# Kernel tuning notes

Measured on AMD Instinct MI355X. Metric: run time of the kernel, lower is better.

The kernel has to match this reference:

```python
import jax, jax.numpy as jnp
import numpy as np


def to_tb(r, size, base=4):
    # (B, size, size, size) -> (B, (size//base)^3, base, base, base)
    n = size // base
    r = r.reshape(-1, size, size, n, base)
    r = r.transpose(0, 1, 3, 2, 4)
    r = r.reshape(-1, size, n * n, base, base)
    r = r.transpose(0, 2, 1, 3, 4)
    return r.reshape(-1, n ** 3, base, base, base)


def from_tb(r, size, base=4):
    # inverse-ish of to_tb, ends with an extra (0,1,3,2) transpose as in source
    n = size // base
    r = r.reshape(-1, n * n, size, base, base)
    r = r.transpose(0, 2, 1, 3, 4)
    r = r.reshape(-1, size, size, n, base)
    r = r.transpose(0, 1, 3, 2, 4)
    r = r.reshape(-1, size, size, size)
    return r.transpose(0, 1, 3, 2)


def downscale(r, size):
    r = to_tb(r, size)  # base=4
    r = r.sum(axis=(2, 3, 4)) / 64.0
    r = r.reshape(-1, size // 4, size // 4, size // 4)
    return r.transpose(0, 3, 2, 1)


def setup_inputs() -> dict:
    key = jax.random.key(0)
    # (batch=2, level=4, 4, 4, 4^(3*4-2)) with 4*4*1048576 = 256^3 per slice
    x = jax.random.normal(key, (2, 4, 4, 4, 1048576), dtype=jnp.float32)
    return {"x": x}


def reference(x):
    level = x.shape[1]
    xt = jnp.transpose(x, (1, 0, 2, 3, 4))  # (level, batch, 4, 4, ...)
    batch = xt.shape[1]
    d2 = xt.shape[2]
    size_full = 4 ** level
    n3 = (4 ** (level - 1)) ** 3
    ret = []
    for i in range(level):
        r = xt[i]
        r = from_tb(r, size_full, 4 ** i)  # -> (batch, size, size, size)
        for k in range(i):
            r = downscale(r, 4 ** (level - k))
        for _ in range(i):
            r = jnp.tile(r, (1, 4, 4, 4))
        r = to_tb(r, size_full)  # (batch, n3, 4, 4, 4)
        ret.append(r.reshape(-1, n3, 64))
    out = jnp.stack(ret)  # (level, batch, n3, 64)
    out = out.transpose(1, 0, 2, 3).reshape(batch, -1, d2 ** 3)
    return out
```

## Files before the change

kernel.cpp:

```cpp
#include <hip/hip_runtime.h>


typedef float f4 __attribute__((ext_vector_type(4)));

__global__ __launch_bounds__(256) void k_reduce(const float* __restrict__ in,
                                                float* __restrict__ d1,
                                                float* __restrict__ p2,
                                                float* __restrict__ p3) {
    const int b = blockIdx.y;
    const int bx = blockIdx.x;
    const int tid = threadIdx.x;
    __shared__ float red[64];
    const f4* in4 = (const f4*)in;

    if (bx < 1024) {
        const int tlow = bx;
        const long base4 = (long)b * 16777216 + 4194304;
        float acc[4] = {0.f, 0.f, 0.f, 0.f};
        for (int dz = 0; dz < 4; ++dz) {
            long rb = base4 + (long)(dz * 1024 + tlow) * 1024;
#pragma unroll
            for (int k = 0; k < 4; ++k) {
                f4 v = __builtin_nontemporal_load(&in4[rb + k * 256 + tid]);
                acc[k] += v.x + v.y + v.z + v.w;
            }
        }
#pragma unroll
        for (int k = 0; k < 4; ++k) {
            acc[k] += __shfl_xor(acc[k], 4);
            acc[k] += __shfl_xor(acc[k], 8);
        }
        if ((tid & 12) == 0) {
            int yp = tlow >> 4;
            int zp = ((tlow & 15) << 2) + (tid & 3);
#pragma unroll
            for (int k = 0; k < 4; ++k) {
                int xp = k * 16 + (tid >> 4);
                int f4i = (zp >> 2) * 4096 + (yp >> 2) * 256 +
                          (xp >> 2) * 16 + (xp & 3) * 4 + (yp & 3);
                d1[b * 262144 + f4i * 4 + (zp & 3)] = acc[k] * (1.0f / 64.0f);
            }
        }
    } else if (bx < 2048) {
        const int blk = bx - 1024;
        const int g = blk & 3, cell = blk >> 2;
        const int yp = cell >> 4, xp = cell & 15;
        const long base4 = (long)b * 16777216 + 2 * 4194304 + yp * 16384 + xp * 1024;
        float acc = 0.f;
        for (int dzi = 0; dzi < 4; ++dzi) {
            long rb = base4 + (long)(g * 4 + dzi) * 262144;
#pragma unroll
            for (int k = 0; k < 4; ++k) {
                f4 v = __builtin_nontemporal_load(&in4[rb + k * 256 + tid]);
                acc += v.x + v.y + v.z + v.w;
            }
        }
        acc += __shfl_xor(acc, 1);
        acc += __shfl_xor(acc, 2);
        if ((tid & 3) == 0) red[tid >> 2] = acc;
        __syncthreads();
        if (tid < 16) {
            float s = red[tid] + red[16 + tid] + red[32 + tid] + red[48 + tid];
            p2[(b * 4 + g) * 4096 + xp * 256 + yp * 16 + tid] = s;
        }
    } else {
        const int blk = bx - 2048;
        const int kc = blk & 3;
        const int orig = blk >> 2;
        const int xp = orig >> 6, hi = (orig >> 2) & 15, dxg = orig & 3;
        const long base4 = (long)b * 16777216 + 3 * 4194304 +
                           (long)hi * 262144 + xp * 65536 + dxg * 16384;
        float acc = 0.f;
        for (int kk = 0; kk < 16; ++kk) {
            f4 v = __builtin_nontemporal_load(&in4[base4 + (kc * 16 + kk) * 256 + tid]);
            acc += v.x + v.y + v.z + v.w;
        }
        acc += __shfl_xor(acc, 1);
        acc += __shfl_xor(acc, 2);
        acc += __shfl_xor(acc, 4);
        acc += __shfl_xor(acc, 8);
        if ((tid & 15) == 0) red[tid >> 4] = acc;
        __syncthreads();
        if (tid < 16) {
            int G = (hi * 4 + dxg) * 4 + kc;
            p3[((b * 4 + xp) * 256 + G) * 16 + tid] = red[tid];
        }
    }
}

__global__ __launch_bounds__(256) void k_write(const float* __restrict__ in,
                                               const float* __restrict__ d1,
                                               const float* __restrict__ p2,
                                               const float* __restrict__ p3,
                                               float* __restrict__ out) {
    const int b = blockIdx.y;
    const int bx = blockIdx.x;
    const int tid = threadIdx.x;
    __shared__ f4 smem4[1040];
    f4* out4 = (f4*)out;

    if (bx < 4096) {
        float* smem = (float*)smem4;
        const f4* in4 = (const f4*)in;
        const int Y_hi = bx >> 6, Z_hi = bx & 63;
        const long in_b4 = (long)b * 16777216;
#pragma unroll
        for (int k = 0; k < 4; ++k) {
            int idx = k * 256 + tid;
            int r = idx >> 6, col4 = idx & 63;
            int Y = Y_hi * 4 + (r >> 2), Z = Z_hi * 4 + (r & 3);
            f4 v = __builtin_nontemporal_load(&in4[in_b4 + (long)Y * 16384 + Z * 64 + col4]);
            *(f4*)&smem[r * 260 + col4 * 4] = v;
        }
        __syncthreads();
        const long out_b4 = (long)b * 16777216 + (long)Z_hi * 65536 + Y_hi * 1024;
#pragma unroll
        for (int k = 0; k < 4; ++k) {
            int idx = k * 256 + tid;
            int X = ((idx >> 4) << 2) + ((tid >> 2) & 3);
            int row0 = (tid & 3) * 4;
            f4 v;
            v.x = smem[(row0 + 0) * 260 + X];
            v.y = smem[(row0 + 1) * 260 + X];
            v.z = smem[(row0 + 2) * 260 + X];
            v.w = smem[(row0 + 3) * 260 + X];
            __builtin_nontemporal_store(v, &out4[out_b4 + idx]);
        }
    } else if (bx < 6144) {
        const int blk = bx - 4096;
        const f4* d14 = (const f4*)d1;
        const int bx0 = blk * 2;
        const int base = b * 65536 + ((bx0 >> 6) & 15) * 4096 + (bx0 & 15) * 256 + tid;
        const f4 v0 = d14[base];
        const f4 v1 = d14[base + 256];
        const long ob = (long)b * 16777216 + 4194304 + (long)blk * 2048;
#pragma unroll
        for (int j = 0; j < 8; ++j)
            __builtin_nontemporal_store((j < 4) ? v0 : v1, &out4[ob + j * 256 + tid]);
    } else if (bx < 8192) {
        const int blk = bx - 6144;
        const f4* p24 = (const f4*)p2;
        const int bx0 = blk * 2;
        const int t6 = tid & 63;
        const int xp = ((t6 >> 4) << 2) + ((t6 >> 2) & 3);
        const int ylo = t6 & 3;
        f4 v01[2];
#pragma unroll
        for (int r = 0; r < 2; ++r) {
            int row = bx0 + r;
            int zq = (row >> 6) & 3, yq = row & 3;
            int yp = yq * 4 + ylo;
            f4 s = {0.f, 0.f, 0.f, 0.f};
#pragma unroll
            for (int g = 0; g < 4; ++g)
                s += p24[(b * 4 + g) * 1024 + xp * 64 + yp * 4 + zq];
            v01[r] = s * (1.0f / 4096.0f);
        }
        const long ob = (long)b * 16777216 + 2 * 4194304 + (long)blk * 2048;
#pragma unroll
        for (int j = 0; j < 8; ++j)
            __builtin_nontemporal_store((j < 4) ? v01[0] : v01[1],
                                        &out4[ob + j * 256 + tid]);
    } else {
        const int blk = bx - 8192;
        const f4* p34 = (const f4*)p3;
        const int o = tid & 15, part = tid >> 4;
        const int xp = o >> 2, cq = o & 3;
        f4 s = {0.f, 0.f, 0.f, 0.f};
#pragma unroll
        for (int j = 0; j < 16; ++j) {
            int G = part * 16 + j;
            s += p34[((b * 4 + xp) * 256 + G) * 4 + cq];
        }
        f4* red = smem4;
        red[part * 16 + o] = s;
        __syncthreads();
        f4* tab = smem4 + 256;
        if (tid < 16) {
            f4 t = {0.f, 0.f, 0.f, 0.f};
#pragma unroll
            for (int g = 0; g < 16; ++g) t += red[g * 16 + tid];
            tab[tid] = t * (1.0f / 262144.0f);
        }
        __syncthreads();
        const f4 v = tab[tid & 15];
        const long ob = (long)b * 16777216 + 3 * 4194304 + (long)blk * 8192;
#pragma unroll
        for (int j = 0; j < 32; ++j)
            __builtin_nontemporal_store(v, &out4[ob + j * 256 + tid]);
    }
}

extern "C" void kernel_launch(void* const* d_in, const int* in_sizes, int n_in,
                              void* d_out, int out_size, void* d_ws, size_t ws_size,
                              hipStream_t stream) {
    const float* in = (const float*)d_in[0];
    float* out = (float*)d_out;
    float* ws = (float*)d_ws;
    float* d1 = ws;
    float* p2 = ws + 524288;
    float* p3 = ws + 524288 + 65536;
    k_reduce<<<dim3(3072, 2), 256, 0, stream>>>(in, d1, p2, p3);
    k_write <<<dim3(8704, 2), 256, 0, stream>>>(in, d1, p2, p3, out);
}
```

Measured before the change: 186.6 us.

## Move level-0 transpose copy into reduce kernel, split broadcast writes into second kernel

The level-0 transpose-copy blocks move from the write kernel into the first kernel, so the whole input-read phase (reductions plus the transposing copy) runs in one launch. The second kernel now holds only the broadcast-fill blocks that read the small partial-sum buffers. The read-heavy and write-heavy work is rebalanced across the two launches, and the biggest broadcast blocks are scheduled first. Reduction blocks are also interleaved by batch instead of using a 2D grid. The cost is a larger shared allocation in the fused first kernel, which may lower its occupancy.

```diff
diff --git a/kernel.cpp b/kernel.cpp
--- a/kernel.cpp
+++ b/kernel.cpp
@@ -3,106 +3,100 @@
 
 typedef float f4 __attribute__((ext_vector_type(4)));
 
-__global__ __launch_bounds__(256) void k_reduce(const float* __restrict__ in,
-                                                float* __restrict__ d1,
-                                                float* __restrict__ p2,
-                                                float* __restrict__ p3) {
-    const int b = blockIdx.y;
+__global__ __launch_bounds__(256) void k_read(const float* __restrict__ in,
+                                              float* __restrict__ out,
+                                              float* __restrict__ d1,
+                                              float* __restrict__ p2,
+                                              float* __restrict__ p3) {
     const int bx = blockIdx.x;
     const int tid = threadIdx.x;
-    __shared__ float red[64];
+    __shared__ float smem[16 * 260];
     const f4* in4 = (const f4*)in;
 
-    if (bx < 1024) {
-        const int tlow = bx;
-        const long base4 = (long)b * 16777216 + 4194304;
-        float acc[4] = {0.f, 0.f, 0.f, 0.f};
-        for (int dz = 0; dz < 4; ++dz) {
-            long rb = base4 + (long)(dz * 1024 + tlow) * 1024;
+    if (bx < 6144) {
+        const int b = bx & 1;
+        const int rbx = bx >> 1;
+        float* red = smem;
+
+        if (rbx < 1024) {
+            const int tlow = rbx;
+            const long base4 = (long)b * 16777216 + 4194304;
+            float acc[4] = {0.f, 0.f, 0.f, 0.f};
+            for (int dz = 0; dz < 4; ++dz) {
+                long rb = base4 + (long)(dz * 1024 + tlow) * 1024;
+#pragma unroll
+                for (int k = 0; k < 4; ++k) {
+                    f4 v = __builtin_nontemporal_load(&in4[rb + k * 256 + tid]);
+                    acc[k] += v.x + v.y + v.z + v.w;
+                }
+            }
 #pragma unroll
             for (int k = 0; k < 4; ++k) {
-                f4 v = __builtin_nontemporal_load(&in4[rb + k * 256 + tid]);
-                acc[k] += v.x + v.y + v.z + v.w;
-            }
-        }
-#pragma unroll
-        for (int k = 0; k < 4; ++k) {
-            acc[k] += __shfl_xor(acc[k], 4);
-            acc[k] += __shfl_xor(acc[k], 8);
-        }
-        if ((tid & 12) == 0) {
-            int yp = tlow >> 4;
-            int zp = ((tlow & 15) << 2) + (tid & 3);
-#pragma unroll
-            for (int k = 0; k < 4; ++k) {
-                int xp = k * 16 + (tid >> 4);
-                int f4i = (zp >> 2) * 4096 + (yp >> 2) * 256 +
-                          (xp >> 2) * 16 + (xp & 3) * 4 + (yp & 3);
-                d1[b * 262144 + f4i * 4 + (zp & 3)] = acc[k] * (1.0f / 64.0f);
-            }
-        }
-    } else if (bx < 2048) {
-        const int blk = bx - 1024;
-        const int g = blk & 3, cell = blk >> 2;
-        const int yp = cell >> 4, xp = cell & 15;
-        const long base4 = (long)b * 16777216 + 2 * 4194304 + yp * 16384 + xp * 1024;
-        float acc = 0.f;
-        for (int dzi = 0; dzi < 4; ++dzi) {
-            long rb = base4 + (long)(g * 4 + dzi) * 262144;
-#pragma unroll
-            for (int k = 0; k < 4; ++k) {
-                f4 v = __builtin_nontemporal_load(&in4[rb + k * 256 + tid]);
+                acc[k] += __shfl_xor(acc[k], 4);
+                acc[k] += __shfl_xor(acc[k], 8);
+            }
+            if ((tid & 12) == 0) {
+                int yp = tlow >> 4;
+                int zp = ((tlow & 15) << 2) + (tid & 3);
+#pragma unroll
+                for (int k = 0; k < 4; ++k) {
+                    int xp = k * 16 + (tid >> 4);
+                    int f4i = (zp >> 2) * 4096 + (yp >> 2) * 256 +
+                              (xp >> 2) * 16 + (xp & 3) * 4 + (yp & 3);
+                    d1[b * 262144 + f4i * 4 + (zp & 3)] = acc[k] * (1.0f / 64.0f);
+                }
+            }
+        } else if (rbx < 2048) {
+            const int blk = rbx - 1024;
+            const int g = blk & 3, cell = blk >> 2;
+            const int yp = cell >> 4, xp = cell & 15;
+            const long base4 = (long)b * 16777216 + 2 * 4194304 + yp * 16384 + xp * 1024;
+            float acc = 0.f;
+            for (int dzi = 0; dzi < 4; ++dzi) {
+                long rb = base4 + (long)(g * 4 + dzi) * 262144;
+#pragma unroll
+                for (int k = 0; k < 4; ++k) {
+                    f4 v = __builtin_nontemporal_load(&in4[rb + k * 256 + tid]);
+                    acc += v.x + v.y + v.z + v.w;
+                }
+            }
+            acc += __shfl_xor(acc, 1);
+            acc += __shfl_xor(acc, 2);
+            if ((tid & 3) == 0) red[tid >> 2] = acc;
+            __syncthreads();
+            if (tid < 16) {
+                float s = red[tid] + red[16 + tid] + red[32 + tid] + red[48 + tid];
+                p2[(b * 4 + g) * 4096 + xp * 256 + yp * 16 + tid] = s;
+            }
+        } else {
+            const int blk = rbx - 2048;
+            const int kc = blk & 3;
+            const int orig = blk >> 2;
+            const int xp = orig >> 6, hi = (orig >> 2) & 15, dxg = orig & 3;
+            const long base4 = (long)b * 16777216 + 3 * 4194304 +
+                               (long)hi * 262144 + xp * 65536 + dxg * 16384;
+            float acc = 0.f;
+            for (int kk = 0; kk < 16; ++kk) {
+                f4 v = __builtin_nontemporal_load(&in4[base4 + (kc * 16 + kk) * 256 + tid]);
                 acc += v.x + v.y + v.z + v.w;
             }
-        }
-        acc += __shfl_xor(acc, 1);
-        acc += __shfl_xor(acc, 2);
-        if ((tid & 3) == 0) red[tid >> 2] = acc;
-        __syncthreads();
-        if (tid < 16) {
-            float s = red[tid] + red[16 + tid] + red[32 + tid] + red[48 + tid];
-            p2[(b * 4 + g) * 4096 + xp * 256 + yp * 16 + tid] = s;
+            acc += __shfl_xor(acc, 1);
+            acc += __shfl_xor(acc, 2);
+            acc += __shfl_xor(acc, 4);
+            acc += __shfl_xor(acc, 8);
+            if ((tid & 15) == 0) red[tid >> 4] = acc;
+            __syncthreads();
+            if (tid < 16) {
+                int G = (hi * 4 + dxg) * 4 + kc;
+                p3[((b * 4 + xp) * 256 + G) * 16 + tid] = red[tid];
+            }
         }
     } else {
-        const int blk = bx - 2048;
-        const int kc = blk & 3;
-        const int orig = blk >> 2;
-        const int xp = orig >> 6, hi = (orig >> 2) & 15, dxg = orig & 3;
-        const long base4 = (long)b * 16777216 + 3 * 4194304 +
-                           (long)hi * 262144 + xp * 65536 + dxg * 16384;
-        float acc = 0.f;
-        for (int kk = 0; kk < 16; ++kk) {
-            f4 v = __builtin_nontemporal_load(&in4[base4 + (kc * 16 + kk) * 256 + tid]);
-            acc += v.x + v.y + v.z + v.w;
-        }
-        acc += __shfl_xor(acc, 1);
-        acc += __shfl_xor(acc, 2);
-        acc += __shfl_xor(acc, 4);
-        acc += __shfl_xor(acc, 8);
-        if ((tid & 15) == 0) red[tid >> 4] = acc;
-        __syncthreads();
-        if (tid < 16) {
-            int G = (hi * 4 + dxg) * 4 + kc;
-            p3[((b * 4 + xp) * 256 + G) * 16 + tid] = red[tid];
-        }
-    }
-}
-
-__global__ __launch_bounds__(256) void k_write(const float* __restrict__ in,
-                                               const float* __restrict__ d1,
-                                               const float* __restrict__ p2,
-                                               const float* __restrict__ p3,
-                                               float* __restrict__ out) {
-    const int b = blockIdx.y;
-    const int bx = blockIdx.x;
-    const int tid = threadIdx.x;
-    __shared__ f4 smem4[1040];
-    f4* out4 = (f4*)out;
-
-    if (bx < 4096) {
-        float* smem = (float*)smem4;
-        const f4* in4 = (const f4*)in;
-        const int Y_hi = bx >> 6, Z_hi = bx & 63;
+        const int p = bx - 6144;
+        const int b = p >> 12;
+        const int rem = p & 4095;
+        const int Y_hi = rem >> 6, Z_hi = rem & 63;
+        f4* out4 = (f4*)out;
         const long in_b4 = (long)b * 16777216;
 #pragma unroll
         for (int k = 0; k < 4; ++k) {
@@ -126,8 +120,48 @@
             v.w = smem[(row0 + 3) * 260 + X];
             __builtin_nontemporal_store(v, &out4[out_b4 + idx]);
         }
-    } else if (bx < 6144) {
-        const int blk = bx - 4096;
+    }
+}
+
+__global__ __launch_bounds__(256) void k_bcast(const float* __restrict__ d1,
+                                               const float* __restrict__ p2,
+                                               const float* __restrict__ p3,
+                                               float* __restrict__ out) {
+    const int b = blockIdx.y;
+    const int bx = blockIdx.x;
+    const int tid = threadIdx.x;
+    __shared__ f4 smem4[280];
+    f4* out4 = (f4*)out;
+
+    if (bx < 512) {
+        const int blk = bx;
+        const f4* p34 = (const f4*)p3;
+        const int o = tid & 15, part = tid >> 4;
+        const int xp = o >> 2, cq = o & 3;
+        f4 s = {0.f, 0.f, 0.f, 0.f};
+#pragma unroll
+        for (int j = 0; j < 16; ++j) {
+            int G = part * 16 + j;
+            s += p34[((b * 4 + xp) * 256 + G) * 4 + cq];
+        }
+        f4* red = smem4;
+        red[part * 16 + o] = s;
+        __syncthreads();
+        f4* tab = smem4 + 256;
+        if (tid < 16) {
+            f4 t = {0.f, 0.f, 0.f, 0.f};
+#pragma unroll
+            for (int g = 0; g < 16; ++g) t += red[g * 16 + tid];
+            tab[tid] = t * (1.0f / 262144.0f);
+        }
+        __syncthreads();
+        const f4 v = tab[tid & 15];
+        const long ob = (long)b * 16777216 + 3 * 4194304 + (long)blk * 8192;
+#pragma unroll
+        for (int j = 0; j < 32; ++j)
+            __builtin_nontemporal_store(v, &out4[ob + j * 256 + tid]);
+    } else if (bx < 2560) {
+        const int blk = bx - 512;
         const f4* d14 = (const f4*)d1;
         const int bx0 = blk * 2;
         const int base = b * 65536 + ((bx0 >> 6) & 15) * 4096 + (bx0 & 15) * 256 + tid;
@@ -137,8 +171,8 @@
 #pragma unroll
         for (int j = 0; j < 8; ++j)
             __builtin_nontemporal_store((j < 4) ? v0 : v1, &out4[ob + j * 256 + tid]);
-    } else if (bx < 8192) {
-        const int blk = bx - 6144;
+    } else {
+        const int blk = bx - 2560;
         const f4* p24 = (const f4*)p2;
         const int bx0 = blk * 2;
         const int t6 = tid & 63;
@@ -161,33 +195,6 @@
         for (int j = 0; j < 8; ++j)
             __builtin_nontemporal_store((j < 4) ? v01[0] : v01[1],
                                         &out4[ob + j * 256 + tid]);
-    } else {
-        const int blk = bx - 8192;
-        const f4* p34 = (const f4*)p3;
-        const int o = tid & 15, part = tid >> 4;
-        const int xp = o >> 2, cq = o & 3;
-        f4 s = {0.f, 0.f, 0.f, 0.f};
-#pragma unroll
-        for (int j = 0; j < 16; ++j) {
-            int G = part * 16 + j;
-            s += p34[((b * 4 + xp) * 256 + G) * 4 + cq];
-        }
-        f4* red = smem4;
-        red[part * 16 + o] = s;
-        __syncthreads();
-        f4* tab = smem4 + 256;
-        if (tid < 16) {
-            f4 t = {0.f, 0.f, 0.f, 0.f};
-#pragma unroll
-            for (int g = 0; g < 16; ++g) t += red[g * 16 + tid];
-            tab[tid] = t * (1.0f / 262144.0f);
-        }
-        __syncthreads();
-        const f4 v = tab[tid & 15];
-        const long ob = (long)b * 16777216 + 3 * 4194304 + (long)blk * 8192;
-#pragma unroll
-        for (int j = 0; j < 32; ++j)
-            __builtin_nontemporal_store(v, &out4[ob + j * 256 + tid]);
     }
 }
 
@@ -200,6 +207,6 @@
     float* d1 = ws;
     float* p2 = ws + 524288;
     float* p3 = ws + 524288 + 65536;
-    k_reduce<<<dim3(3072, 2), 256, 0, stream>>>(in, d1, p2, p3);
-    k_write <<<dim3(8704, 2), 256, 0, stream>>>(in, d1, p2, p3, out);
+    k_read <<<dim3(14336),   256, 0, stream>>>(in, out, d1, p2, p3);
+    k_bcast<<<dim3(4608, 2), 256, 0, stream>>>(d1, p2, p3, out);
 }
```

Measured after the change: 181.9 us. 1.03x faster.
